# Kernel optimization log

Hardware: AMD Instinct MI355X
Metric: run time of the kernel (lower is better)

Reference implementation:

```python
import jax, jax.numpy as jnp
import numpy as np
from jax import lax

B = 2_000_000


def _conv1d(x, w, stride):
    # x: [B, Cin, L], w: [Cout, Cin, K] (torch Conv1d layout)
    return lax.conv_general_dilated(x, w, window_strides=(stride,), padding='VALID',
                                    dimension_numbers=('NCH', 'OIH', 'NCH'))


def _deconv1d(x, w, stride):
    # x: [B, Cin, L], w: [Cin, Cout, K] (torch ConvTranspose1d layout)
    return lax.conv_transpose(x, w, strides=(stride,), padding='VALID',
                              dimension_numbers=('NCH', 'IOH', 'NCH'),
                              transpose_kernel=True)


def setup_inputs() -> dict:
    key = jax.random.key(0)
    ks = jax.random.split(key, 13)
    s = 0.5
    return {
        'x': jax.random.normal(ks[0], (B, 18), dtype=jnp.float32),
        'fc_obs_w': jax.random.normal(ks[1], (2, 4), dtype=jnp.float32) * s,
        'fc_obs_b': jax.random.normal(ks[2], (2,), dtype=jnp.float32) * s,
        'fc_emb_w': jax.random.normal(ks[3], (2, 2), dtype=jnp.float32) * s,
        'fc_emb_b': jax.random.normal(ks[4], (2,), dtype=jnp.float32) * s,
        'conv1_w': jax.random.normal(ks[5], (1, 2, 3), dtype=jnp.float32) * s,
        'conv1_b': jax.random.normal(ks[6], (1,), dtype=jnp.float32) * s,
        'conv2_w': jax.random.normal(ks[7], (1, 1, 2), dtype=jnp.float32) * s,
        'conv2_b': jax.random.normal(ks[8], (1,), dtype=jnp.float32) * s,
        'deconv1_w': jax.random.normal(ks[9], (1, 1, 2), dtype=jnp.float32) * s,
        'deconv1_b': jax.random.normal(ks[10], (1,), dtype=jnp.float32) * s,
        'deconv2_w': jax.random.normal(ks[11], (1, 1, 3), dtype=jnp.float32) * s,
        'deconv2_b': jax.random.normal(ks[12], (1,), dtype=jnp.float32) * s,
    }


def reference(x, fc_obs_w, fc_obs_b, fc_emb_w, fc_emb_b,
              conv1_w, conv1_b, conv2_w, conv2_b,
              deconv1_w, deconv1_b, deconv2_w, deconv2_b):
    obs = x[:, :4]                     # [B,4]
    j = x[:, 4:11]                     # [B,7]
    jd = x[:, 11:18]                   # [B,7]
    jcat = jnp.stack([j, jd], axis=1)  # [B,2,7] (conv1 in_channels=2)

    fc_obs = jax.nn.relu(obs @ fc_obs_w.T + fc_obs_b)            # [B,2]

    fm = jax.nn.relu(_conv1d(jcat, conv1_w, 2) + conv1_b[None, :, None])   # [B,1,3]
    fm = jax.nn.relu(_conv1d(fm, conv2_w, 1) + conv2_b[None, :, None])     # [B,1,2]
    fm = fm[:, 0, :]                                                        # [B,2]

    fc_emb = jax.nn.relu((fc_obs + fm) @ fc_emb_w.T + fc_emb_b)  # [B,2]
    fc_emb = fc_emb[:, None, :]                                  # [B,1,2]

    fm = jax.nn.relu(_deconv1d(fc_emb, deconv1_w, 1) + deconv1_b[None, :, None])  # [B,1,3]
    out = _deconv1d(fm, deconv2_w, 2) + deconv2_b[None, :, None]                  # [B,1,7]
    return out
```

## Files before the change

### kernel.cpp

```cpp
#include <hip/hip_runtime.h>

#define TPB 256

__global__ __launch_bounds__(TPB) void conv_policy_kernel(
    const float* __restrict__ x,
    const float* __restrict__ fow,
    const float* __restrict__ fob,
    const float* __restrict__ few,
    const float* __restrict__ feb,
    const float* __restrict__ w1,
    const float* __restrict__ b1,
    const float* __restrict__ w2,
    const float* __restrict__ b2,
    const float* __restrict__ dw1,
    const float* __restrict__ db1,
    const float* __restrict__ dw2,
    const float* __restrict__ db2,
    float* __restrict__ out,
    int n)
{
    __shared__ __align__(16) float lds[TPB * 18];
    const int tid  = threadIdx.x;
    const int base = blockIdx.x * TPB;
    const bool full = (base + TPB) <= n;

    if (full) {
        const float4* src = (const float4*)(x + (size_t)base * 18);
        float4*       dst = (float4*)lds;
        #pragma unroll
        for (int k = 0; k < 5; ++k) {
            int idx = k * TPB + tid;
            if (idx < (TPB * 18) / 4) dst[idx] = src[idx];
        }
    } else {
        const int total = n * 18;
        #pragma unroll
        for (int k = 0; k < 18; ++k) {
            int idx = k * TPB + tid;
            int g   = base * 18 + idx;
            if (g < total) lds[idx] = x[g];
        }
    }
    __syncthreads();

    float r[18];
    #pragma unroll
    for (int i = 0; i < 18; ++i) r[i] = lds[tid * 18 + i];

    const float b1v = b1[0], b2v = b2[0], db1v = db1[0], db2v = db2[0];
    const float w10 = w1[0], w11 = w1[1], w12 = w1[2], w13 = w1[3], w14 = w1[4], w15 = w1[5];
    const float w20 = w2[0], w21 = w2[1];
    const float dw10 = dw1[0], dw11 = dw1[1];
    const float dw20 = dw2[0], dw21 = dw2[1], dw22 = dw2[2];

    float fo0 = fmaxf(r[0]*fow[0] + r[1]*fow[1] + r[2]*fow[2] + r[3]*fow[3] + fob[0], 0.f);
    float fo1 = fmaxf(r[0]*fow[4] + r[1]*fow[5] + r[2]*fow[6] + r[3]*fow[7] + fob[1], 0.f);

    float c1[3];
    #pragma unroll
    for (int p = 0; p < 3; ++p) {
        float s = r[4  + 2*p] * w10 + r[5  + 2*p] * w11 + r[6  + 2*p] * w12
                + r[11 + 2*p] * w13 + r[12 + 2*p] * w14 + r[13 + 2*p] * w15 + b1v;
        c1[p] = fmaxf(s, 0.f);
    }

    float c20 = fmaxf(c1[0]*w20 + c1[1]*w21 + b2v, 0.f);
    float c21 = fmaxf(c1[1]*w20 + c1[2]*w21 + b2v, 0.f);

    float t0 = fo0 + c20, t1 = fo1 + c21;
    float e0 = fmaxf(t0*few[0] + t1*few[1] + feb[0], 0.f);
    float e1 = fmaxf(t0*few[2] + t1*few[3] + feb[1], 0.f);

    float d0 = fmaxf(e0*dw10 + db1v, 0.f);
    float d1 = fmaxf(e0*dw11 + e1*dw10 + db1v, 0.f);
    float d2 = fmaxf(e1*dw11 + db1v, 0.f);

    float o[7];
    o[0] = d0*dw20 + db2v;
    o[1] = d0*dw21 + db2v;
    o[2] = d0*dw22 + d1*dw20 + db2v;
    o[3] = d1*dw21 + db2v;
    o[4] = d1*dw22 + d2*dw20 + db2v;
    o[5] = d2*dw21 + db2v;
    o[6] = d2*dw22 + db2v;

    __syncthreads();
    #pragma unroll
    for (int q = 0; q < 7; ++q) lds[tid * 7 + q] = o[q];
    __syncthreads();

    if (full) {
        float4*       dst = (float4*)(out + (size_t)base * 7);
        const float4* src = (const float4*)lds;
        #pragma unroll
        for (int k = 0; k < 2; ++k) {
            int idx = k * TPB + tid;
            if (idx < (TPB * 7) / 4) dst[idx] = src[idx];
        }
    } else {
        const int total = n * 7;
        #pragma unroll
        for (int k = 0; k < 7; ++k) {
            int idx = k * TPB + tid;
            int g   = base * 7 + idx;
            if (g < total) out[g] = lds[idx];
        }
    }
}

extern "C" void kernel_launch(void* const* d_in, const int* in_sizes, int n_in,
                              void* d_out, int out_size, void* d_ws, size_t ws_size,
                              hipStream_t stream) {
    const float* x   = (const float*)d_in[0];
    const float* fow = (const float*)d_in[1];
    const float* fob = (const float*)d_in[2];
    const float* few = (const float*)d_in[3];
    const float* feb = (const float*)d_in[4];
    const float* w1  = (const float*)d_in[5];
    const float* b1  = (const float*)d_in[6];
    const float* w2  = (const float*)d_in[7];
    const float* b2  = (const float*)d_in[8];
    const float* dw1 = (const float*)d_in[9];
    const float* db1 = (const float*)d_in[10];
    const float* dw2 = (const float*)d_in[11];
    const float* db2 = (const float*)d_in[12];
    float* out = (float*)d_out;

    const int n    = in_sizes[0] / 18;
    const int grid = (n + TPB - 1) / TPB;
    conv_policy_kernel<<<grid, TPB, 0, stream>>>(
        x, fow, fob, few, feb, w1, b1, w2, b2, dw1, db1, dw2, db2, out, n);
}
```

Before: 243.8 us.

## Stage input per-wave via direct global-to-LDS loads and drop block barriers

Each 64-row wave now loads its own slice of the input straight into LDS using global_load_lds, so the data skips the register round trip, and block-wide __syncthreads are replaced by per-wave waitcnt and wave barriers. Outputs are written with nontemporal vector stores, and the weight scalar loads are issued while the async loads are in flight. This targets barrier stalls and extra instruction overhead in a memory-bound kernel. It relies on hand-coded waitcnt encodings and LDS layout assumptions that are tied to the hardware.

After: 241.6 us. About the same (-0.9%).

```diff
diff --git a/kernel.cpp b/kernel.cpp
--- a/kernel.cpp
+++ b/kernel.cpp
@@ -2,108 +2,131 @@
 
 #define TPB 256
 
-__global__ __launch_bounds__(TPB) void conv_policy_kernel(
-    const float* __restrict__ x,
-    const float* __restrict__ fow,
-    const float* __restrict__ fob,
-    const float* __restrict__ few,
-    const float* __restrict__ feb,
-    const float* __restrict__ w1,
-    const float* __restrict__ b1,
-    const float* __restrict__ w2,
-    const float* __restrict__ b2,
-    const float* __restrict__ dw1,
-    const float* __restrict__ db1,
-    const float* __restrict__ dw2,
-    const float* __restrict__ db2,
-    float* __restrict__ out,
-    int n)
-{
-    __shared__ __align__(16) float lds[TPB * 18];
-    const int tid  = threadIdx.x;
-    const int base = blockIdx.x * TPB;
-    const bool full = (base + TPB) <= n;
+typedef float v4f __attribute__((ext_vector_type(4)));
 
-    if (full) {
-        const float4* src = (const float4*)(x + (size_t)base * 18);
-        float4*       dst = (float4*)lds;
-        #pragma unroll
-        for (int k = 0; k < 5; ++k) {
-            int idx = k * TPB + tid;
-            if (idx < (TPB * 18) / 4) dst[idx] = src[idx];
-        }
-    } else {
-        const int total = n * 18;
-        #pragma unroll
-        for (int k = 0; k < 18; ++k) {
-            int idx = k * TPB + tid;
-            int g   = base * 18 + idx;
-            if (g < total) lds[idx] = x[g];
-        }
-    }
-    __syncthreads();
+#define WAITCNT_VM0   0x0F70
+#define WAITCNT_LGKM0 0xC07F
 
-    float r[18];
-    #pragma unroll
-    for (int i = 0; i < 18; ++i) r[i] = lds[tid * 18 + i];
+struct Wts {
+    float fow0,fow1,fow2,fow3,fow4,fow5,fow6,fow7,fob0,fob1;
+    float few0,few1,few2,few3,feb0,feb1;
+    float w10,w11,w12,w13,w14,w15,b1v,b2v;
+    float w20,w21,dw10,dw11,db1v,db2v,dw20,dw21,dw22;
+};
 
-    const float b1v = b1[0], b2v = b2[0], db1v = db1[0], db2v = db2[0];
-    const float w10 = w1[0], w11 = w1[1], w12 = w1[2], w13 = w1[3], w14 = w1[4], w15 = w1[5];
-    const float w20 = w2[0], w21 = w2[1];
-    const float dw10 = dw1[0], dw11 = dw1[1];
-    const float dw20 = dw2[0], dw21 = dw2[1], dw22 = dw2[2];
-
-    float fo0 = fmaxf(r[0]*fow[0] + r[1]*fow[1] + r[2]*fow[2] + r[3]*fow[3] + fob[0], 0.f);
-    float fo1 = fmaxf(r[0]*fow[4] + r[1]*fow[5] + r[2]*fow[6] + r[3]*fow[7] + fob[1], 0.f);
-
+__device__ __forceinline__ void compute_row(const float r[18], const Wts& W, float o[7]) {
+    float fo0 = fmaxf(r[0]*W.fow0 + r[1]*W.fow1 + r[2]*W.fow2 + r[3]*W.fow3 + W.fob0, 0.f);
+    float fo1 = fmaxf(r[0]*W.fow4 + r[1]*W.fow5 + r[2]*W.fow6 + r[3]*W.fow7 + W.fob1, 0.f);
     float c1[3];
     #pragma unroll
     for (int p = 0; p < 3; ++p) {
-        float s = r[4  + 2*p] * w10 + r[5  + 2*p] * w11 + r[6  + 2*p] * w12
-                + r[11 + 2*p] * w13 + r[12 + 2*p] * w14 + r[13 + 2*p] * w15 + b1v;
+        float s = r[4  + 2*p]*W.w10 + r[5  + 2*p]*W.w11 + r[6  + 2*p]*W.w12
+                + r[11 + 2*p]*W.w13 + r[12 + 2*p]*W.w14 + r[13 + 2*p]*W.w15 + W.b1v;
         c1[p] = fmaxf(s, 0.f);
     }
+    float c20 = fmaxf(c1[0]*W.w20 + c1[1]*W.w21 + W.b2v, 0.f);
+    float c21 = fmaxf(c1[1]*W.w20 + c1[2]*W.w21 + W.b2v, 0.f);
+    float t0 = fo0 + c20, t1 = fo1 + c21;
+    float e0 = fmaxf(t0*W.few0 + t1*W.few1 + W.feb0, 0.f);
+    float e1 = fmaxf(t0*W.few2 + t1*W.few3 + W.feb1, 0.f);
+    float d0 = fmaxf(e0*W.dw10 + W.db1v, 0.f);
+    float d1 = fmaxf(e0*W.dw11 + e1*W.dw10 + W.db1v, 0.f);
+    float d2 = fmaxf(e1*W.dw11 + W.db1v, 0.f);
+    o[0] = d0*W.dw20 + W.db2v;
+    o[1] = d0*W.dw21 + W.db2v;
+    o[2] = d0*W.dw22 + d1*W.dw20 + W.db2v;
+    o[3] = d1*W.dw21 + W.db2v;
+    o[4] = d1*W.dw22 + d2*W.dw20 + W.db2v;
+    o[5] = d2*W.dw21 + W.db2v;
+    o[6] = d2*W.dw22 + W.db2v;
+}
 
-    float c20 = fmaxf(c1[0]*w20 + c1[1]*w21 + b2v, 0.f);
-    float c21 = fmaxf(c1[1]*w20 + c1[2]*w21 + b2v, 0.f);
+__global__ __launch_bounds__(TPB) void conv_policy_kernel(
+    const float* __restrict__ x,
+    const float* __restrict__ fow, const float* __restrict__ fob,
+    const float* __restrict__ few, const float* __restrict__ feb,
+    const float* __restrict__ w1,  const float* __restrict__ b1,
+    const float* __restrict__ w2,  const float* __restrict__ b2,
+    const float* __restrict__ dw1, const float* __restrict__ db1,
+    const float* __restrict__ dw2, const float* __restrict__ db2,
+    float* __restrict__ out, int n)
+{
+    __shared__ __align__(16) float lds[TPB * 18];
+    const int tid     = threadIdx.x;
+    const int lane    = tid & 63;
+    const int wave    = tid >> 6;
+    const int base    = blockIdx.x * TPB;
+    const int rowbase = base + wave * 64;
 
-    float t0 = fo0 + c20, t1 = fo1 + c21;
-    float e0 = fmaxf(t0*few[0] + t1*few[1] + feb[0], 0.f);
-    float e1 = fmaxf(t0*few[2] + t1*few[3] + feb[1], 0.f);
+    if (rowbase >= n) return;
 
-    float d0 = fmaxf(e0*dw10 + db1v, 0.f);
-    float d1 = fmaxf(e0*dw11 + e1*dw10 + db1v, 0.f);
-    float d2 = fmaxf(e1*dw11 + db1v, 0.f);
+    const bool wfull = (rowbase + 64) <= n;
 
-    float o[7];
-    o[0] = d0*dw20 + db2v;
-    o[1] = d0*dw21 + db2v;
-    o[2] = d0*dw22 + d1*dw20 + db2v;
-    o[3] = d1*dw21 + db2v;
-    o[4] = d1*dw22 + d2*dw20 + db2v;
-    o[5] = d2*dw21 + db2v;
-    o[6] = d2*dw22 + db2v;
+    float* ldsw = lds + wave * 1152;
 
-    __syncthreads();
-    #pragma unroll
-    for (int q = 0; q < 7; ++q) lds[tid * 7 + q] = o[q];
-    __syncthreads();
+    if (wfull) {
+        const float4* src4 = (const float4*)(x + (size_t)rowbase * 18);
+        #pragma unroll
+        for (int k = 0; k < 4; ++k) {
+            __builtin_amdgcn_global_load_lds(
+                (const __attribute__((address_space(1))) void*)(src4 + k * 64 + lane),
+                (__attribute__((address_space(3))) void*)(ldsw + k * 256),
+                16, 0, 0);
+        }
+        if (lane < 32) {
+            __builtin_amdgcn_global_load_lds(
+                (const __attribute__((address_space(1))) void*)(src4 + 256 + lane),
+                (__attribute__((address_space(3))) void*)(ldsw + 1024),
+                16, 0, 0);
+        }
+    }
 
-    if (full) {
-        float4*       dst = (float4*)(out + (size_t)base * 7);
-        const float4* src = (const float4*)lds;
+    Wts W;
+    W.fow0=fow[0];W.fow1=fow[1];W.fow2=fow[2];W.fow3=fow[3];
+    W.fow4=fow[4];W.fow5=fow[5];W.fow6=fow[6];W.fow7=fow[7];
+    W.fob0=fob[0];W.fob1=fob[1];
+    W.few0=few[0];W.few1=few[1];W.few2=few[2];W.few3=few[3];
+    W.feb0=feb[0];W.feb1=feb[1];
+    W.w10=w1[0];W.w11=w1[1];W.w12=w1[2];W.w13=w1[3];W.w14=w1[4];W.w15=w1[5];
+    W.b1v=b1[0];W.b2v=b2[0];
+    W.w20=w2[0];W.w21=w2[1];
+    W.dw10=dw1[0];W.dw11=dw1[1];W.db1v=db1[0];W.db2v=db2[0];
+    W.dw20=dw2[0];W.dw21=dw2[1];W.dw22=dw2[2];
+
+    if (wfull) {
+        __builtin_amdgcn_s_waitcnt(WAITCNT_VM0);
+        __builtin_amdgcn_wave_barrier();
+
+        float r[18];
+        const float2* rowp = (const float2*)(ldsw + lane * 18);
         #pragma unroll
-        for (int k = 0; k < 2; ++k) {
-            int idx = k * TPB + tid;
-            if (idx < (TPB * 7) / 4) dst[idx] = src[idx];
-        }
+        for (int i = 0; i < 9; ++i) { float2 v = rowp[i]; r[2*i] = v.x; r[2*i+1] = v.y; }
+
+        float o[7];
+        compute_row(r, W, o);
+
+        __builtin_amdgcn_s_waitcnt(WAITCNT_LGKM0);
+        __builtin_amdgcn_wave_barrier();
+        #pragma unroll
+        for (int q = 0; q < 7; ++q) ldsw[lane * 7 + q] = o[q];
+        __builtin_amdgcn_s_waitcnt(WAITCNT_LGKM0);
+        __builtin_amdgcn_wave_barrier();
+
+        v4f*       dst  = (v4f*)(out + (size_t)rowbase * 7);
+        const v4f* vsrc = (const v4f*)ldsw;
+        __builtin_nontemporal_store(vsrc[lane], dst + lane);
+        if (lane < 48)
+            __builtin_nontemporal_store(vsrc[64 + lane], dst + 64 + lane);
     } else {
-        const int total = n * 7;
-        #pragma unroll
-        for (int k = 0; k < 7; ++k) {
-            int idx = k * TPB + tid;
-            int g   = base * 7 + idx;
-            if (g < total) out[g] = lds[idx];
+        int row = rowbase + lane;
+        if (row < n) {
+            float r[18];
+            #pragma unroll
+            for (int i = 0; i < 18; ++i) r[i] = x[(size_t)row * 18 + i];
+            float o[7];
+            compute_row(r, W, o);
+            #pragma unroll
+            for (int q = 0; q < 7; ++q) out[(size_t)row * 7 + q] = o[q];
         }
     }
 }
```
